# Kernel tuning notes

Measured on AMD Instinct MI355X. Metric: run time of the kernel, lower is better.

Reference implementation:

```python
import math
import jax, jax.numpy as jnp
from jax import lax
import numpy as np

B, Q, D, H = 64, 512, 128, 256
KS, BLOCKS = 3, 2
PI = math.pi

def _ln(x, w, b):
    m = x.mean(-1, keepdims=True)
    v = ((x - m) ** 2).mean(-1, keepdims=True)
    return (x - m) / jnp.sqrt(v + 1e-5) * w + b

def _conv1d(x, w, b, dil):
    # x: (B, C, L), w: (O, I, K), replicate ('edge') padding as in torch padding_mode='replicate'
    pad = (w.shape[-1] - 1) * dil // 2
    xp = jnp.pad(x, ((0, 0), (0, 0), (pad, pad)), mode='edge')
    y = lax.conv_general_dilated(xp, w, (1,), 'VALID', rhs_dilation=(dil,),
                                 dimension_numbers=('NCH', 'OIH', 'NCH'))
    return y + b[None, :, None]

def _rotate(x, rho, phi):
    M = x.shape[-1] // 2
    re, im = x[:, :M], x[:, M:]
    c, s = jnp.cos(phi), jnp.sin(phi)
    return jnp.concatenate([rho * (c * re - s * im), rho * (s * re + c * im)], axis=1)

def setup_inputs():
    key = jax.random.key(0)
    ks = iter(jax.random.split(key, 40))
    def nrm(shape, scale=0.05):
        return jax.random.normal(next(ks), shape, dtype=jnp.float32) * scale
    inp = {}
    inp['x_in'] = jax.random.normal(next(ks), (B, Q, D), dtype=jnp.float32)
    inp['w_out'] = 64
    inp['inp_w'] = nrm((H, 3 * D, 1)); inp['inp_b'] = jnp.zeros((H,), jnp.float32)
    for i in range(BLOCKS):
        inp['blk%d_c1_w' % i] = nrm((H, H, KS)); inp['blk%d_c1_b' % i] = jnp.zeros((H,), jnp.float32)
        inp['blk%d_c2_w' % i] = nrm((H, H, KS)); inp['blk%d_c2_b' % i] = jnp.zeros((H,), jnp.float32)
        inp['blk%d_ln_w' % i] = jnp.ones((H,), jnp.float32); inp['blk%d_ln_b' % i] = jnp.zeros((H,), jnp.float32)
    inp['out_ln_w'] = jnp.ones((H,), jnp.float32); inp['out_ln_b'] = jnp.zeros((H,), jnp.float32)
    inp['fc_gain_w'] = nrm((D, H)); inp['fc_gain_b'] = jnp.zeros((D,), jnp.float32)
    inp['fc_rp_w'] = nrm((2, H)); inp['fc_rp_b'] = jnp.zeros((2,), jnp.float32)
    inp['roll_in_w'] = nrm((H, H + D)); inp['roll_in_b'] = jnp.zeros((H,), jnp.float32)
    inp['gru_w_ih'] = nrm((3 * H, H)); inp['gru_w_hh'] = nrm((3 * H, H))
    inp['gru_b_ih'] = jnp.zeros((3 * H,), jnp.float32); inp['gru_b_hh'] = jnp.zeros((3 * H,), jnp.float32)
    inp['roll_ln_w'] = jnp.ones((H,), jnp.float32); inp['roll_ln_b'] = jnp.zeros((H,), jnp.float32)
    inp['fc_rp_r_w'] = nrm((2, H)); inp['fc_rp_r_b'] = jnp.zeros((2,), jnp.float32)
    return inp

def reference(x_in, w_out, inp_w, inp_b,
              blk0_c1_w, blk0_c1_b, blk0_c2_w, blk0_c2_b, blk0_ln_w, blk0_ln_b,
              blk1_c1_w, blk1_c1_b, blk1_c2_w, blk1_c2_b, blk1_ln_w, blk1_ln_b,
              out_ln_w, out_ln_b, fc_gain_w, fc_gain_b, fc_rp_w, fc_rp_b,
              roll_in_w, roll_in_b, gru_w_ih, gru_w_hh, gru_b_ih, gru_b_hh,
              roll_ln_w, roll_ln_b, fc_rp_r_w, fc_rp_r_b):
    # ---- feature construction: [y, dy, ddy] with dy[0]=ddy[0]=0, ddy[1]=dy[1]
    dy = jnp.concatenate([jnp.zeros_like(x_in[:, :1]), x_in[:, 1:] - x_in[:, :-1]], axis=1)
    ddy = jnp.concatenate([jnp.zeros_like(dy[:, :1]), dy[:, 1:] - dy[:, :-1]], axis=1)
    feats = jnp.concatenate([x_in, dy, ddy], axis=-1)  # (B, q, 3D)
    # ---- TCN encoder (eval mode: dropout = identity)
    h = _conv1d(feats.transpose(0, 2, 1), inp_w, inp_b, 1)  # (B, H, q)
    blks = [(blk0_c1_w, blk0_c1_b, blk0_c2_w, blk0_c2_b, blk0_ln_w, blk0_ln_b, 1),
            (blk1_c1_w, blk1_c1_b, blk1_c2_w, blk1_c2_b, blk1_ln_w, blk1_ln_b, 2)]
    for c1w, c1b, c2w, c2b, lnw, lnb, dil in blks:
        y = jax.nn.gelu(_conv1d(h, c1w, c1b, dil), approximate=False)
        y = jax.nn.gelu(_conv1d(y, c2w, c2b, dil), approximate=False)
        h = _ln((h + y).transpose(0, 2, 1), lnw, lnb).transpose(0, 2, 1)
    h_seq = _ln(h.transpose(0, 2, 1), out_ln_w, out_ln_b)  # (B, q, H)
    # ---- Kalman-style rotate/gain recurrence over q steps
    def kstep(x_post, inputs):
        y_t, h_t = inputs
        rp = h_t @ fc_rp_w.T + fc_rp_b
        rho = jax.nn.sigmoid(rp[:, 0:1]) * 1.25
        phi = PI * jnp.tanh(rp[:, 1:2])
        x_pri = _rotate(x_post, rho, phi)
        Kg = jax.nn.sigmoid(h_t @ fc_gain_w.T + fc_gain_b)
        return x_pri + Kg * (y_t - x_pri), None
    x_post, _ = lax.scan(kstep, x_in[:, 0, :],
                         (x_in.transpose(1, 0, 2), h_seq.transpose(1, 0, 2)))
    # ---- GRU rollout for w_out steps (torch GRUCell gate order: r|z|n)
    def gru(zx, hh):
        gi = zx @ gru_w_ih.T + gru_b_ih
        gh = hh @ gru_w_hh.T + gru_b_hh
        ir, iz, inn = jnp.split(gi, 3, axis=-1)
        hr, hz, hn = jnp.split(gh, 3, axis=-1)
        r = jax.nn.sigmoid(ir + hr)
        zg = jax.nn.sigmoid(iz + hz)
        n = jnp.tanh(inn + r * hn)
        return (1.0 - zg) * n + zg * hh
    def rstep(carry, _):
        h_r, curr = carry
        z = jnp.tanh(jnp.concatenate([h_r, curr], axis=1) @ roll_in_w.T + roll_in_b)
        h_r = _ln(gru(z, h_r), roll_ln_w, roll_ln_b)
        rp = h_r @ fc_rp_r_w.T + fc_rp_r_b
        rho = jax.nn.sigmoid(rp[:, 0:1]) * 1.25
        phi = PI * jnp.tanh(rp[:, 1:2])
        curr = _rotate(curr, rho, phi)
        return (h_r, curr), curr
    _, preds = lax.scan(rstep, (h_seq[:, -1, :], x_post), None, length=w_out)
    return preds.transpose(1, 0, 2)  # (B, w_out, D)
```

## Files before the change

### kernel.cpp

```cpp
#include <hip/hip_runtime.h>
#include <math.h>

#define QLEN 512
#define NB   64
#define DD   128
#define HH   256
#define WOUT 64
#define PI_F 3.14159265358979323846f

typedef __attribute__((ext_vector_type(8))) short bf16x8;
typedef __attribute__((ext_vector_type(4))) float f32x4;

__device__ __forceinline__ float sigmf(float x){ return 1.0f/(1.0f+expf(-x)); }
__device__ __forceinline__ float geluf(float x){ return 0.5f*x*(1.0f+erff(x*0.7071067811865476f)); }

__device__ __forceinline__ unsigned short f2bf(float f){
    unsigned u = __float_as_uint(f);
    u += 0x7fffu + ((u >> 16) & 1u);
    return (unsigned short)(u >> 16);
}
__device__ __forceinline__ float bf2f(unsigned short h){
    return __uint_as_float(((unsigned)h) << 16);
}

__device__ __forceinline__ void packw_elem(const float* __restrict__ w,
                                           unsigned short* __restrict__ dst,
                                           int idx, int CIN, int COUT, int KS) {
    int j = idx & 7; int rest = idx >> 3;
    int lane = rest & 63; rest >>= 6;
    int NT = COUT >> 4;
    int nt = rest % NT; int kt = rest / NT;
    int k = kt*32 + (lane >> 4)*8 + j;
    int cout = nt*16 + (lane & 15);
    int tap = k / CIN, ci = k - tap*CIN;
    float v = w[((size_t)cout*CIN + ci)*KS + tap];
    unsigned short h0 = f2bf(v);  float r = v - bf2f(h0);
    unsigned short h1 = f2bf(r);  r -= bf2f(h1);
    unsigned short h2 = f2bf(r);
    int SZ = KS*CIN*COUT;
    dst[idx] = h0; dst[SZ + idx] = h1; dst[2*SZ + idx] = h2;
}
__device__ __forceinline__ void pq_elem(const float* __restrict__ in,
                                        float4* __restrict__ out,
                                        int idx, int R, int C) {
    int r = idx % R, j4 = idx / R;
    const float* p = in + (size_t)r*C + 4*j4;
    float4 v; v.x = p[0]; v.y = p[1]; v.z = p[2]; v.w = p[3];
    out[idx] = v;
}
__global__ __launch_bounds__(256) void prep_k(
    const float* __restrict__ inp_w, const float* __restrict__ b0c1w,
    const float* __restrict__ b0c2w, const float* __restrict__ b1c1w,
    const float* __restrict__ b1c2w, const float* __restrict__ gainw,
    const float* __restrict__ riw,  const float* __restrict__ wih,
    const float* __restrict__ whh,
    unsigned short* __restrict__ Pinp,  unsigned short* __restrict__ Pb0c1,
    unsigned short* __restrict__ Pb0c2, unsigned short* __restrict__ Pb1c1,
    unsigned short* __restrict__ Pb1c2, unsigned short* __restrict__ Pgain,
    float4* __restrict__ Wri4, float4* __restrict__ Wih4, float4* __restrict__ Whh4)
{
    int idx = blockIdx.x*256 + threadIdx.x;
    if      (idx <   98304) packw_elem(inp_w, Pinp,  idx,          384, 256, 1);
    else if (idx <  294912) packw_elem(b0c1w, Pb0c1, idx -  98304, 256, 256, 3);
    else if (idx <  491520) packw_elem(b0c2w, Pb0c2, idx - 294912, 256, 256, 3);
    else if (idx <  688128) packw_elem(b1c1w, Pb1c1, idx - 491520, 256, 256, 3);
    else if (idx <  884736) packw_elem(b1c2w, Pb1c2, idx - 688128, 256, 256, 3);
    else if (idx <  917504) packw_elem(gainw, Pgain, idx - 884736, 256, 128, 1);
    else if (idx <  942080) pq_elem(riw, Wri4, idx - 917504, 256, 384);
    else if (idx <  991232) pq_elem(wih, Wih4, idx - 942080, 768, 256);
    else if (idx < 1040384) pq_elem(whh, Whh4, idx - 991232, 768, 256);
}

template<int CIN, int COUT, int KS, int DIL, int ACT, int FEATS, int TM>
__global__ __launch_bounds__(256, 2) void conv_mfma_k(
    const float* __restrict__ X, const unsigned short* __restrict__ W,
    const float* __restrict__ bias, float* __restrict__ Y)
{
    constexpr int HALO = (KS == 3) ? DIL : 0;
    constexpr int ROWS = TM + 2*HALO;
    constexpr int CINP = CIN + 8;
    constexpr int MF   = TM/16;
    constexpr int NF   = COUT/64;
    constexpr int KT   = (KS*CIN)/32;
    constexpr int TPC  = CIN/32;
    constexpr int WSZ  = KS*CIN*COUT;

    __shared__ __align__(16) unsigned short As[3][ROWS][CINP];

    const int b   = blockIdx.y;
    const int t0  = blockIdx.x * TM;
    const int tid = threadIdx.x;

    if constexpr (FEATS) {
        for (int idx = tid; idx < TM*DD; idx += 256) {
            int r = idx >> 7, d = idx & (DD-1);
            int t = t0 + r;
            const float* xr = X + ((size_t)b*QLEN + t)*DD + d;
            float x    = xr[0];
            float xm1  = (t >= 1) ? xr[-DD]   : 0.f;
            float xm2  = (t >= 2) ? xr[-2*DD] : 0.f;
            float dy   = (t >= 1) ? (x - xm1)   : 0.f;
            float dym1 = (t >= 2) ? (xm1 - xm2) : 0.f;
            float ddy  = (t >= 1) ? (dy - dym1) : 0.f;
            float vals[3] = {x, dy, ddy};
            #pragma unroll
            for (int f = 0; f < 3; ++f) {
                float v = vals[f];
                unsigned short h0 = f2bf(v);  float rr = v - bf2f(h0);
                unsigned short h1 = f2bf(rr); rr -= bf2f(h1);
                unsigned short h2 = f2bf(rr);
                As[0][r][f*DD + d] = h0;
                As[1][r][f*DD + d] = h1;
                As[2][r][f*DD + d] = h2;
            }
        }
    } else {
        for (int idx = tid; idx < ROWS*(CIN/4); idx += 256) {
            int r = idx / (CIN/4), c4 = idx % (CIN/4);
            int gr = t0 + r - HALO;
            gr = gr < 0 ? 0 : (gr > QLEN-1 ? QLEN-1 : gr);
            float4 v = reinterpret_cast<const float4*>(X + ((size_t)b*QLEN + gr)*CIN)[c4];
            float vv[4] = {v.x, v.y, v.z, v.w};
            ushort4 s0, s1, s2;
            unsigned short* q0 = (unsigned short*)&s0;
            unsigned short* q1 = (unsigned short*)&s1;
            unsigned short* q2 = (unsigned short*)&s2;
            #pragma unroll
            for (int e = 0; e < 4; ++e) {
                float v1 = vv[e];
                unsigned short h0 = f2bf(v1);  float rr = v1 - bf2f(h0);
                unsigned short h1 = f2bf(rr);  rr -= bf2f(h1);
                q0[e] = h0; q1[e] = h1; q2[e] = f2bf(rr);
            }
            *reinterpret_cast<ushort4*>(&As[0][r][c4*4]) = s0;
            *reinterpret_cast<ushort4*>(&As[1][r][c4*4]) = s1;
            *reinterpret_cast<ushort4*>(&As[2][r][c4*4]) = s2;
        }
    }
    __syncthreads();

    const int wv = tid >> 6, l = tid & 63;
    const int lr = l & 15, lk = l >> 4;

    f32x4 acc[MF][NF];
    #pragma unroll
    for (int m = 0; m < MF; ++m)
        #pragma unroll
        for (int n = 0; n < NF; ++n)
            #pragma unroll
            for (int i = 0; i < 4; ++i) acc[m][n][i] = 0.f;

    auto loadB = [&](int kt, bf16x8 (&Bf)[NF][3]) {
        #pragma unroll
        for (int n = 0; n < NF; ++n) {
            const unsigned short* p =
                W + ((size_t)(kt*(COUT/16) + wv*NF + n)*64 + l)*8;
            #pragma unroll
            for (int q = 0; q < 3; ++q)
                Bf[n][q] = *reinterpret_cast<const bf16x8*>(p + (size_t)q*WSZ);
        }
    };
    auto comp = [&](int kt, bf16x8 (&Bf)[NF][3]) {
        const int tap = kt / TPC;
        const int kin = (kt % TPC)*32 + lk*8;
        bf16x8 A[MF][3];
        #pragma unroll
        for (int m = 0; m < MF; ++m) {
            const int row = m*16 + lr + tap*DIL;
            #pragma unroll
            for (int q = 0; q < 3; ++q)
                A[m][q] = *reinterpret_cast<const bf16x8*>(&As[q][row][kin]);
        }
        #pragma unroll
        for (int m = 0; m < MF; ++m)
            #pragma unroll
            for (int n = 0; n < NF; ++n) {
                f32x4 c = acc[m][n];
                c = __builtin_amdgcn_mfma_f32_16x16x32_bf16(A[m][0], Bf[n][0], c, 0,0,0);
                c = __builtin_amdgcn_mfma_f32_16x16x32_bf16(A[m][0], Bf[n][1], c, 0,0,0);
                c = __builtin_amdgcn_mfma_f32_16x16x32_bf16(A[m][1], Bf[n][0], c, 0,0,0);
                c = __builtin_amdgcn_mfma_f32_16x16x32_bf16(A[m][0], Bf[n][2], c, 0,0,0);
                c = __builtin_amdgcn_mfma_f32_16x16x32_bf16(A[m][1], Bf[n][1], c, 0,0,0);
                c = __builtin_amdgcn_mfma_f32_16x16x32_bf16(A[m][2], Bf[n][0], c, 0,0,0);
                acc[m][n] = c;
            }
    };

    bf16x8 B0[NF][3], B1[NF][3];
    loadB(0, B0);
    #pragma unroll 1
    for (int kt = 0; kt < KT; kt += 2) {
        loadB(kt+1, B1);
        comp(kt, B0);
        if (kt + 2 < KT) loadB(kt+2, B0);
        comp(kt+1, B1);
    }

    #pragma unroll
    for (int n = 0; n < NF; ++n) {
        const int col = (wv*NF + n)*16 + lr;
        const float bv = bias[col];
        #pragma unroll
        for (int m = 0; m < MF; ++m) {
            #pragma unroll
            for (int i = 0; i < 4; ++i) {
                float v = acc[m][n][i] + bv;
                if constexpr (ACT == 1) v = geluf(v);
                if constexpr (ACT == 2) v = sigmf(v);
                Y[((size_t)b*QLEN + t0 + m*16 + lk*4 + i)*COUT + col] = v;
            }
        }
    }
}

__global__ __launch_bounds__(256) void ln_k(
    const float* __restrict__ X, const float* __restrict__ R,
    const float* __restrict__ w, const float* __restrict__ b,
    float* __restrict__ Y)
{
    int row  = blockIdx.x*4 + (threadIdx.x >> 6);
    int lane = threadIdx.x & 63;
    float4 v = reinterpret_cast<const float4*>(X + (size_t)row*HH)[lane];
    float4 rv = reinterpret_cast<const float4*>(R + (size_t)row*HH)[lane];
    v.x += rv.x; v.y += rv.y; v.z += rv.z; v.w += rv.w;
    float s = v.x + v.y + v.z + v.w;
    #pragma unroll
    for (int off = 32; off > 0; off >>= 1) s += __shfl_xor(s, off);
    float m = s * (1.0f/HH);
    float dx=v.x-m, dy=v.y-m, dz=v.z-m, dw=v.w-m;
    float q = dx*dx + dy*dy + dz*dz + dw*dw;
    #pragma unroll
    for (int off = 32; off > 0; off >>= 1) q += __shfl_xor(q, off);
    float inv = rsqrtf(q*(1.0f/HH) + 1e-5f);
    float4 wv = reinterpret_cast<const float4*>(w)[lane];
    float4 bv = reinterpret_cast<const float4*>(b)[lane];
    float4 o;
    o.x = dx*inv*wv.x + bv.x;
    o.y = dy*inv*wv.y + bv.y;
    o.z = dz*inv*wv.z + bv.z;
    o.w = dw*inv*wv.w + bv.w;
    reinterpret_cast<float4*>(Y + (size_t)row*HH)[lane] = o;
}

__global__ __launch_bounds__(256) void ln_rp_k(
    const float* __restrict__ X, const float* __restrict__ w, const float* __restrict__ b,
    const float* __restrict__ rpw, const float* __restrict__ rpb,
    float* __restrict__ Y, float* __restrict__ rho, float* __restrict__ phi)
{
    int row  = blockIdx.x*4 + (threadIdx.x >> 6);
    int lane = threadIdx.x & 63;
    float4 v = reinterpret_cast<const float4*>(X + (size_t)row*HH)[lane];
    float s = v.x + v.y + v.z + v.w;
    #pragma unroll
    for (int off = 32; off > 0; off >>= 1) s += __shfl_xor(s, off);
    float m = s * (1.0f/HH);
    float dx=v.x-m, dy=v.y-m, dz=v.z-m, dw=v.w-m;
    float q = dx*dx + dy*dy + dz*dz + dw*dw;
    #pragma unroll
    for (int off = 32; off > 0; off >>= 1) q += __shfl_xor(q, off);
    float inv = rsqrtf(q*(1.0f/HH) + 1e-5f);
    float4 wv = reinterpret_cast<const float4*>(w)[lane];
    float4 bv = reinterpret_cast<const float4*>(b)[lane];
    float4 o;
    o.x = dx*inv*wv.x + bv.x;
    o.y = dy*inv*wv.y + bv.y;
    o.z = dz*inv*wv.z + bv.z;
    o.w = dw*inv*wv.w + bv.w;
    reinterpret_cast<float4*>(Y + (size_t)row*HH)[lane] = o;

    float4 w0 = reinterpret_cast<const float4*>(rpw)[lane];
    float4 w1 = reinterpret_cast<const float4*>(rpw + HH)[lane];
    float d0 = o.x*w0.x + o.y*w0.y + o.z*w0.z + o.w*w0.w;
    float d1 = o.x*w1.x + o.y*w1.y + o.z*w1.z + o.w*w1.w;
    #pragma unroll
    for (int off = 32; off > 0; off >>= 1) { d0 += __shfl_xor(d0, off); d1 += __shfl_xor(d1, off); }
    if (lane == 0) {
        rho[row] = 1.25f * sigmf(d0 + rpb[0]);
        phi[row] = PI_F * tanhf(d1 + rpb[1]);
    }
}

__global__ __launch_bounds__(64) void kalman_k(
    const float* __restrict__ Xin, const float* __restrict__ Kg,
    const float* __restrict__ rho_a, const float* __restrict__ phi_a,
    float* __restrict__ xpost)
{
    int b = blockIdx.x, l = threadIdx.x;
    const float* xb = Xin + (size_t)b*QLEN*DD;
    float re = xb[l], im = xb[64 + l];

    float rho_c = rho_a[b*QLEN], phi_c = phi_a[b*QLEN];
    const float* kg0 = Kg + (size_t)b*QLEN*DD;
    float kr_c = kg0[l], ki_c = kg0[64 + l];
    float y0_c = xb[l],  y1_c = xb[64 + l];

    for (int t = 0; t < QLEN; ++t) {
        float rho_n = 0.f, phi_n = 0.f, kr_n = 0.f, ki_n = 0.f, y0_n = 0.f, y1_n = 0.f;
        if (t + 1 < QLEN) {
            rho_n = rho_a[b*QLEN + t + 1];
            phi_n = phi_a[b*QLEN + t + 1];
            const float* kg = Kg + ((size_t)b*QLEN + t + 1)*DD;
            const float* yr = xb + (size_t)(t + 1)*DD;
            kr_n = kg[l]; ki_n = kg[64 + l];
            y0_n = yr[l]; y1_n = yr[64 + l];
        }
        float sn, cs; sincosf(phi_c, &sn, &cs);
        float pr = rho_c*(cs*re - sn*im);
        float pi = rho_c*(sn*re + cs*im);
        re = pr + kr_c*(y0_c - pr);
        im = pi + ki_c*(y1_c - pi);
        rho_c = rho_n; phi_c = phi_n; kr_c = kr_n; ki_c = ki_n; y0_c = y0_n; y1_c = y1_n;
    }
    xpost[b*DD + l]      = re;
    xpost[b*DD + 64 + l] = im;
}

__device__ __forceinline__ float bsum16(float v, float* red) {
    #pragma unroll
    for (int off = 32; off > 0; off >>= 1) v += __shfl_xor(v, off);
    __syncthreads();
    if ((threadIdx.x & 63) == 0) red[threadIdx.x >> 6] = v;
    __syncthreads();
    float s = 0.f;
    #pragma unroll
    for (int i = 0; i < 16; ++i) s += red[i];
    return s;
}
__device__ __forceinline__ float2 bsum16_2(float a, float b, float* red) {
    #pragma unroll
    for (int off = 32; off > 0; off >>= 1) { a += __shfl_xor(a, off); b += __shfl_xor(b, off); }
    __syncthreads();
    if ((threadIdx.x & 63) == 0) { red[threadIdx.x >> 6] = a; red[16 + (threadIdx.x >> 6)] = b; }
    __syncthreads();
    float sa = 0.f, sb = 0.f;
    #pragma unroll
    for (int i = 0; i < 16; ++i) { sa += red[i]; sb += red[16 + i]; }
    float2 r; r.x = sa; r.y = sb; return r;
}

__global__ __launch_bounds__(1024) void rollout_k5(
    const float* __restrict__ Hs, const float* __restrict__ xpost,
    const float4* __restrict__ Wri4,
    const float* __restrict__ rib,
    const float4* __restrict__ Wih4,
    const float4* __restrict__ Whh4,
    const float* __restrict__ bih, const float* __restrict__ bhh,
    const float* __restrict__ lnw, const float* __restrict__ lnb,
    const float* __restrict__ rpw, const float* __restrict__ rpb,
    float* __restrict__ out)
{
    __shared__ __align__(16) float hc[384];
    __shared__ __align__(16) float zsh[256];
    __shared__ float zpart[4][256];
    __shared__ float gpart[6][4][256];
    __shared__ float red[32];

    const int tid = threadIdx.x;
    const int o = tid & 255, p = tid >> 8;
    const int b = blockIdx.x;

    if (p == 0) hc[o] = Hs[((size_t)b*QLEN + QLEN-1)*HH + o];
    if (p == 1 && o < DD) hc[HH + o] = xpost[b*DD + o];

    const float bi0 = bih[o],    bi1 = bih[HH+o], bi2 = bih[2*HH+o];
    const float bh0 = bhh[o],    bh1 = bhh[HH+o], bh2 = bhh[2*HH+o];
    const float rb  = rib[o];
    const float lw  = lnw[o],    lb  = lnb[o];
    const float rw0 = rpw[o],    rw1 = rpw[HH+o];
    const float rpb0 = rpb[0],   rpb1 = rpb[1];
    const float4* hc4 = reinterpret_cast<const float4*>(hc);
    const float4* zf4 = reinterpret_cast<const float4*>(zsh);
    __syncthreads();

    for (int s = 0; s < WOUT; ++s) {
        float az = 0.f;
        {
            const float4* wp = Wri4 + (size_t)(p*24)*256 + o;
            #pragma unroll 8
            for (int j4 = 0; j4 < 24; ++j4) {
                float4 w = wp[(size_t)j4*256];
                float4 h = hc4[p*24 + j4];
                az = fmaf(w.x, h.x, az); az = fmaf(w.y, h.y, az);
                az = fmaf(w.z, h.z, az); az = fmaf(w.w, h.w, az);
            }
        }
        float e0=0.f, e1=0.f, e2=0.f;
        {
            const float4* whp = Whh4 + (size_t)(p*16)*768 + o;
            #pragma unroll 4
            for (int j4 = 0; j4 < 16; ++j4) {
                float4 h = hc4[p*16 + j4];
                float4 wd = whp[(size_t)j4*768];
                float4 we = whp[(size_t)j4*768 + 256];
                float4 wf = whp[(size_t)j4*768 + 512];
                e0 = fmaf(wd.x,h.x,e0); e0 = fmaf(wd.y,h.y,e0); e0 = fmaf(wd.z,h.z,e0); e0 = fmaf(wd.w,h.w,e0);
                e1 = fmaf(we.x,h.x,e1); e1 = fmaf(we.y,h.y,e1); e1 = fmaf(we.z,h.z,e1); e1 = fmaf(we.w,h.w,e1);
                e2 = fmaf(wf.x,h.x,e2); e2 = fmaf(wf.y,h.y,e2); e2 = fmaf(wf.z,h.z,e2); e2 = fmaf(wf.w,h.w,e2);
            }
        }
        zpart[p][o] = az;
        gpart[3][p][o]=e0; gpart[4][p][o]=e1; gpart[5][p][o]=e2;
        __syncthreads();
        if (p == 0)
            zsh[o] = tanhf(zpart[0][o]+zpart[1][o]+zpart[2][o]+zpart[3][o] + rb);
        __syncthreads();

        float g0=0.f, g1=0.f, g2=0.f;
        {
            const float4* wip = Wih4 + (size_t)(p*16)*768 + o;
            #pragma unroll 4
            for (int j4 = 0; j4 < 16; ++j4) {
                float4 z = zf4[p*16 + j4];
                float4 wa = wip[(size_t)j4*768];
                float4 wb = wip[(size_t)j4*768 + 256];
                float4 wc = wip[(size_t)j4*768 + 512];
                g0 = fmaf(wa.x,z.x,g0); g0 = fmaf(wa.y,z.y,g0); g0 = fmaf(wa.z,z.z,g0); g0 = fmaf(wa.w,z.w,g0);
                g1 = fmaf(wb.x,z.x,g1); g1 = fmaf(wb.y,z.y,g1); g1 = fmaf(wb.z,z.z,g1); g1 = fmaf(wb.w,z.w,g1);
                g2 = fmaf(wc.x,z.x,g2); g2 = fmaf(wc.y,z.y,g2); g2 = fmaf(wc.z,z.z,g2); g2 = fmaf(wc.w,z.w,g2);
            }
        }
        gpart[0][p][o]=g0; gpart[1][p][o]=g1; gpart[2][p][o]=g2;
        __syncthreads();

        float go = 0.f;
        if (p == 0) {
            float G0 = gpart[0][0][o]+gpart[0][1][o]+gpart[0][2][o]+gpart[0][3][o] + bi0;
            float G1 = gpart[1][0][o]+gpart[1][1][o]+gpart[1][2][o]+gpart[1][3][o] + bi1;
            float G2 = gpart[2][0][o]+gpart[2][1][o]+gpart[2][2][o]+gpart[2][3][o] + bi2;
            float E0 = gpart[3][0][o]+gpart[3][1][o]+gpart[3][2][o]+gpart[3][3][o] + bh0;
            float E1 = gpart[4][0][o]+gpart[4][1][o]+gpart[4][2][o]+gpart[4][3][o] + bh1;
            float E2 = gpart[5][0][o]+gpart[5][1][o]+gpart[5][2][o]+gpart[5][3][o] + bh2;
            float r  = sigmf(G0 + E0);
            float zg = sigmf(G1 + E1);
            float n  = tanhf(G2 + r*E2);
            go = (1.0f - zg)*n + zg*hc[o];
        }

        float m   = bsum16(go, red) * (1.0f/HH);
        float d   = (p == 0) ? (go - m) : 0.f;
        float var = bsum16(d*d, red) * (1.0f/HH);
        float hn  = (p == 0) ? (d * rsqrtf(var + 1e-5f) * lw + lb) : 0.f;

        float2 ps = bsum16_2((p == 0) ? hn*rw0 : 0.f, (p == 0) ? hn*rw1 : 0.f, red);
        float rho = 1.25f * sigmf(ps.x + rpb0);
        float phi = PI_F * tanhf(ps.y + rpb1);
        float sn, cs; sincosf(phi, &sn, &cs);

        if (p == 0) hc[o] = hn;
        if (tid < 64) {
            float cre = hc[HH + tid], cim = hc[HH + 64 + tid];
            float nr = rho*(cs*cre - sn*cim);
            float ni = rho*(sn*cre + cs*cim);
            hc[HH + tid] = nr; hc[HH + 64 + tid] = ni;
            float* ob = out + ((size_t)b*WOUT + s)*DD;
            ob[tid] = nr; ob[64 + tid] = ni;
        }
        __syncthreads();
    }
}

extern "C" void kernel_launch(void* const* d_in, const int* in_sizes, int n_in,
                              void* d_out, int out_size, void* d_ws, size_t ws_size,
                              hipStream_t stream)
{
    const float* x_in   = (const float*)d_in[0];
    const float* inp_w  = (const float*)d_in[2];
    const float* inp_b  = (const float*)d_in[3];
    const float* b0c1w  = (const float*)d_in[4];
    const float* b0c1b  = (const float*)d_in[5];
    const float* b0c2w  = (const float*)d_in[6];
    const float* b0c2b  = (const float*)d_in[7];
    const float* b0lnw  = (const float*)d_in[8];
    const float* b0lnb  = (const float*)d_in[9];
    const float* b1c1w  = (const float*)d_in[10];
    const float* b1c1b  = (const float*)d_in[11];
    const float* b1c2w  = (const float*)d_in[12];
    const float* b1c2b  = (const float*)d_in[13];
    const float* b1lnw  = (const float*)d_in[14];
    const float* b1lnb  = (const float*)d_in[15];
    const float* olnw   = (const float*)d_in[16];
    const float* olnb   = (const float*)d_in[17];
    const float* gainw  = (const float*)d_in[18];
    const float* gainb  = (const float*)d_in[19];
    const float* rpw    = (const float*)d_in[20];
    const float* rpb    = (const float*)d_in[21];
    const float* riw    = (const float*)d_in[22];
    const float* rib    = (const float*)d_in[23];
    const float* wih    = (const float*)d_in[24];
    const float* whh    = (const float*)d_in[25];
    const float* bih    = (const float*)d_in[26];
    const float* bhh    = (const float*)d_in[27];
    const float* rlnw   = (const float*)d_in[28];
    const float* rlnb   = (const float*)d_in[29];
    const float* rprw   = (const float*)d_in[30];
    const float* rprb   = (const float*)d_in[31];
    float* out = (float*)d_out;

    float* ws   = (float*)d_ws;
    float* buf0 = ws;
    float* buf1 = ws +  8388608;
    float* buf2 = ws + 16777216;
    float* Kg    = buf2;
    float* rhoA  = buf2 + 4194304;
    float* phiA  = rhoA + 32768;
    float* xpost = phiA + 32768;
    float* wts   = ws + 25165824;
    unsigned short* Pinp  = (unsigned short*)wts;
    unsigned short* Pb0c1 = Pinp  + 294912;
    unsigned short* Pb0c2 = Pb0c1 + 589824;
    unsigned short* Pb1c1 = Pb0c2 + 589824;
    unsigned short* Pb1c2 = Pb1c1 + 589824;
    unsigned short* Pgain = Pb1c2 + 589824;
    float4* Wri4 = (float4*)(wts + 1376256);
    float4* Wih4 = (float4*)(wts + 1376256 +  98304);
    float4* Whh4 = (float4*)(wts + 1376256 + 294912);

    prep_k<<<4064, 256, 0, stream>>>(inp_w, b0c1w, b0c2w, b1c1w, b1c2w, gainw,
                                     riw, wih, whh,
                                     Pinp, Pb0c1, Pb0c2, Pb1c1, Pb1c2, Pgain,
                                     Wri4, Wih4, Whh4);

    dim3 cg16(QLEN/16, NB);
    dim3 cg32(QLEN/32, NB);

    conv_mfma_k<384,256,1,1,0,1,16><<<cg16, 256, 0, stream>>>(x_in, Pinp, inp_b, buf0);

    conv_mfma_k<256,256,3,1,1,0,32><<<cg32, 256, 0, stream>>>(buf0, Pb0c1, b0c1b, buf1);
    conv_mfma_k<256,256,3,1,1,0,32><<<cg32, 256, 0, stream>>>(buf1, Pb0c2, b0c2b, buf2);
    ln_k<<<NB*QLEN/4, 256, 0, stream>>>(buf0, buf2, b0lnw, b0lnb, buf1);

    conv_mfma_k<256,256,3,2,1,0,32><<<cg32, 256, 0, stream>>>(buf1, Pb1c1, b1c1b, buf0);
    conv_mfma_k<256,256,3,2,1,0,32><<<cg32, 256, 0, stream>>>(buf0, Pb1c2, b1c2b, buf2);
    ln_k<<<NB*QLEN/4, 256, 0, stream>>>(buf1, buf2, b1lnw, b1lnb, buf0);

    ln_rp_k<<<NB*QLEN/4, 256, 0, stream>>>(buf0, olnw, olnb, rpw, rpb,
                                           buf1, rhoA, phiA);

    conv_mfma_k<256,128,1,1,2,0,32><<<cg32, 256, 0, stream>>>(buf1, Pgain, gainb, Kg);

    kalman_k<<<NB, 64, 0, stream>>>(x_in, Kg, rhoA, phiA, xpost);

    rollout_k5<<<NB, 1024, 0, stream>>>(buf1, xpost, Wri4, rib, Wih4, Whh4,
                                        bih, bhh, rlnw, rlnb, rprw, rprb, out);
}
```

Baseline: 1.714 ms.

## Split GRU rollout across 128 blocks with LDS-resident weight slices and grid barriers

The rollout kernel previously ran one block per batch row and streamed all GRU and input-projection weights from global memory on every step. It now uses 4 groups of 32 blocks. Each block keeps an 8-output slice of the weights in shared memory and serves 16 batch rows, exchanging z and raw h through global buffers. Software grid barriers built on atomic counters (zeroed in prep_k) synchronise each group twice per step. This removes the repeated weight traffic, but it depends on all 128 blocks being co-resident and adds global-barrier latency on every one of the 64 steps.

Result: slower. 2.299 ms (+34.1%).

```diff
diff --git a/kernel.cpp b/kernel.cpp
--- a/kernel.cpp
+++ b/kernel.cpp
@@ -40,24 +40,14 @@
     int SZ = KS*CIN*COUT;
     dst[idx] = h0; dst[SZ + idx] = h1; dst[2*SZ + idx] = h2;
 }
-__device__ __forceinline__ void pq_elem(const float* __restrict__ in,
-                                        float4* __restrict__ out,
-                                        int idx, int R, int C) {
-    int r = idx % R, j4 = idx / R;
-    const float* p = in + (size_t)r*C + 4*j4;
-    float4 v; v.x = p[0]; v.y = p[1]; v.z = p[2]; v.w = p[3];
-    out[idx] = v;
-}
 __global__ __launch_bounds__(256) void prep_k(
     const float* __restrict__ inp_w, const float* __restrict__ b0c1w,
     const float* __restrict__ b0c2w, const float* __restrict__ b1c1w,
     const float* __restrict__ b1c2w, const float* __restrict__ gainw,
-    const float* __restrict__ riw,  const float* __restrict__ wih,
-    const float* __restrict__ whh,
     unsigned short* __restrict__ Pinp,  unsigned short* __restrict__ Pb0c1,
     unsigned short* __restrict__ Pb0c2, unsigned short* __restrict__ Pb1c1,
     unsigned short* __restrict__ Pb1c2, unsigned short* __restrict__ Pgain,
-    float4* __restrict__ Wri4, float4* __restrict__ Wih4, float4* __restrict__ Whh4)
+    unsigned* __restrict__ bars)
 {
     int idx = blockIdx.x*256 + threadIdx.x;
     if      (idx <   98304) packw_elem(inp_w, Pinp,  idx,          384, 256, 1);
@@ -66,9 +56,7 @@
     else if (idx <  688128) packw_elem(b1c1w, Pb1c1, idx - 491520, 256, 256, 3);
     else if (idx <  884736) packw_elem(b1c2w, Pb1c2, idx - 688128, 256, 256, 3);
     else if (idx <  917504) packw_elem(gainw, Pgain, idx - 884736, 256, 128, 1);
-    else if (idx <  942080) pq_elem(riw, Wri4, idx - 917504, 256, 384);
-    else if (idx <  991232) pq_elem(wih, Wih4, idx - 942080, 768, 256);
-    else if (idx < 1040384) pq_elem(whh, Whh4, idx - 991232, 768, 256);
+    else if (idx <  917632) bars[idx - 917504] = 0u;
 }
 
 template<int CIN, int COUT, int KS, int DIL, int ACT, int FEATS, int TM>
@@ -315,147 +303,198 @@
     xpost[b*DD + 64 + l] = im;
 }
 
-__device__ __forceinline__ float bsum16(float v, float* red) {
-    #pragma unroll
-    for (int off = 32; off > 0; off >>= 1) v += __shfl_xor(v, off);
+#define GBLK 32
+#define BPG  16
+#define ZSL  8
+#define GSL  24
+
+__device__ __forceinline__ void gbar(unsigned* cnt, unsigned target) {
     __syncthreads();
-    if ((threadIdx.x & 63) == 0) red[threadIdx.x >> 6] = v;
+    if (threadIdx.x == 0) {
+        unsigned a = __hip_atomic_fetch_add(cnt, 1u, __ATOMIC_ACQ_REL, __HIP_MEMORY_SCOPE_AGENT);
+        if (a != target - 1u) {
+            while (__hip_atomic_load(cnt, __ATOMIC_ACQUIRE, __HIP_MEMORY_SCOPE_AGENT) < target)
+                __builtin_amdgcn_s_sleep(2);
+        }
+    }
     __syncthreads();
-    float s = 0.f;
-    #pragma unroll
-    for (int i = 0; i < 16; ++i) s += red[i];
-    return s;
-}
-__device__ __forceinline__ float2 bsum16_2(float a, float b, float* red) {
-    #pragma unroll
-    for (int off = 32; off > 0; off >>= 1) { a += __shfl_xor(a, off); b += __shfl_xor(b, off); }
-    __syncthreads();
-    if ((threadIdx.x & 63) == 0) { red[threadIdx.x >> 6] = a; red[16 + (threadIdx.x >> 6)] = b; }
-    __syncthreads();
-    float sa = 0.f, sb = 0.f;
-    #pragma unroll
-    for (int i = 0; i < 16; ++i) { sa += red[i]; sb += red[16 + i]; }
-    float2 r; r.x = sa; r.y = sb; return r;
-}
-
-__global__ __launch_bounds__(1024) void rollout_k5(
+}
+
+__global__ __launch_bounds__(1024) void rollout_k7(
     const float* __restrict__ Hs, const float* __restrict__ xpost,
-    const float4* __restrict__ Wri4,
-    const float* __restrict__ rib,
-    const float4* __restrict__ Wih4,
-    const float4* __restrict__ Whh4,
+    const float* __restrict__ riw, const float* __restrict__ rib,
+    const float* __restrict__ wih, const float* __restrict__ whh,
     const float* __restrict__ bih, const float* __restrict__ bhh,
     const float* __restrict__ lnw, const float* __restrict__ lnb,
     const float* __restrict__ rpw, const float* __restrict__ rpb,
-    float* __restrict__ out)
-{
-    __shared__ __align__(16) float hc[384];
-    __shared__ __align__(16) float zsh[256];
-    __shared__ float zpart[4][256];
-    __shared__ float gpart[6][4][256];
-    __shared__ float red[32];
+    float* __restrict__ zbuf, float* __restrict__ hraw,
+    unsigned* __restrict__ bars, float* __restrict__ out)
+{
+    __shared__ __align__(16) float Wri_s[ZSL][388];
+    __shared__ __align__(16) float Wih_s[GSL][260];
+    __shared__ __align__(16) float Whh_s[GSL][260];
+    __shared__ __align__(16) float hcs[BPG][388];
+    __shared__ __align__(16) float sbuf[BPG][260];
+    __shared__ float ghs[GSL][BPG];
+    __shared__ float gis[GSL][BPG];
+    __shared__ float lnw_s[256], lnb_s[256], rw0_s[256], rw1_s[256];
 
     const int tid = threadIdx.x;
-    const int o = tid & 255, p = tid >> 8;
-    const int b = blockIdx.x;
-
-    if (p == 0) hc[o] = Hs[((size_t)b*QLEN + QLEN-1)*HH + o];
-    if (p == 1 && o < DD) hc[HH + o] = xpost[b*DD + o];
-
-    const float bi0 = bih[o],    bi1 = bih[HH+o], bi2 = bih[2*HH+o];
-    const float bh0 = bhh[o],    bh1 = bhh[HH+o], bh2 = bhh[2*HH+o];
-    const float rb  = rib[o];
-    const float lw  = lnw[o],    lb  = lnb[o];
-    const float rw0 = rpw[o],    rw1 = rpw[HH+o];
-    const float rpb0 = rpb[0],   rpb1 = rpb[1];
-    const float4* hc4 = reinterpret_cast<const float4*>(hc);
-    const float4* zf4 = reinterpret_cast<const float4*>(zsh);
+    const int g   = blockIdx.x >> 5;
+    const int j   = blockIdx.x & 31;
+    const int o0  = j * ZSL;
+    const int b0  = g * BPG;
+    unsigned* bcnt = bars + g*32;
+
+    for (int i = tid; i < ZSL*384; i += 1024) {
+        int r = i / 384, k = i - r*384;
+        Wri_s[r][k] = riw[(size_t)(o0 + r)*384 + k];
+    }
+    for (int i = tid; i < GSL*256; i += 1024) {
+        int r = i >> 8, k = i & 255;
+        int gate = r >> 3, oo = r & 7;
+        size_t grow = (size_t)(gate*256 + o0 + oo)*256 + k;
+        Wih_s[r][k] = wih[grow];
+        Whh_s[r][k] = whh[grow];
+    }
+    if (tid < 256) {
+        lnw_s[tid] = lnw[tid]; lnb_s[tid] = lnb[tid];
+        rw0_s[tid] = rpw[tid]; rw1_s[tid] = rpw[256 + tid];
+    }
+    for (int i = tid; i < BPG*256; i += 1024) {
+        int b = i >> 8, c = i & 255;
+        hcs[b][c] = Hs[((size_t)(b0 + b)*QLEN + (QLEN-1))*HH + c];
+    }
+    for (int i = tid; i < BPG*128; i += 1024) {
+        int b = i >> 7, c = i & 127;
+        hcs[b][256 + c] = xpost[(b0 + b)*DD + c];
+    }
+
+    const int zoo = tid & 7, zb2 = tid >> 3;
+    const int u   = tid - 64;
+    const int gbt = (u >= 0) ? (u / 24) : 0;
+    const int gr  = (u >= 0) ? (u - gbt*24) : 0;
+    const int bbt = tid / 24, br = tid - bbt*24;
+    float ribv = 0.f, bhhv = 0.f, bihv = 0.f;
+    if (tid < 64)               ribv = rib[o0 + zoo];
+    if (tid >= 64 && tid < 160) bhhv = bhh[(gr >> 3)*256 + o0 + (gr & 7)];
+    if (tid < 96)               bihv = bih[(br >> 3)*256 + o0 + (br & 7)];
+    const float rpb0 = rpb[0], rpb1 = rpb[1];
     __syncthreads();
 
-    for (int s = 0; s < WOUT; ++s) {
-        float az = 0.f;
+    unsigned nbar = 0;
+
+    for (int s = 0; ; ++s) {
+        if (s > 0) {
+            {
+                int b = tid >> 6, c4 = tid & 63;
+                *reinterpret_cast<float4*>(&sbuf[b][c4*4]) =
+                    *reinterpret_cast<const float4*>(hraw + (size_t)(b0 + b)*256 + c4*4);
+            }
+            __syncthreads();
+            {
+                const int b = tid >> 6, l = tid & 63;
+                float4 v = *reinterpret_cast<const float4*>(&sbuf[b][l*4]);
+                float sm = v.x + v.y + v.z + v.w;
+                #pragma unroll
+                for (int off = 32; off > 0; off >>= 1) sm += __shfl_xor(sm, off);
+                float m = sm * (1.0f/HH);
+                float dx=v.x-m, dy=v.y-m, dz=v.z-m, dw=v.w-m;
+                float q = dx*dx + dy*dy + dz*dz + dw*dw;
+                #pragma unroll
+                for (int off = 32; off > 0; off >>= 1) q += __shfl_xor(q, off);
+                float inv = rsqrtf(q*(1.0f/HH) + 1e-5f);
+                float h0 = dx*inv*lnw_s[l*4+0] + lnb_s[l*4+0];
+                float h1 = dy*inv*lnw_s[l*4+1] + lnb_s[l*4+1];
+                float h2 = dz*inv*lnw_s[l*4+2] + lnb_s[l*4+2];
+                float h3 = dw*inv*lnw_s[l*4+3] + lnb_s[l*4+3];
+                float4 hv; hv.x=h0; hv.y=h1; hv.z=h2; hv.w=h3;
+                *reinterpret_cast<float4*>(&hcs[b][l*4]) = hv;
+                float d0 = h0*rw0_s[l*4+0] + h1*rw0_s[l*4+1] + h2*rw0_s[l*4+2] + h3*rw0_s[l*4+3];
+                float d1 = h0*rw1_s[l*4+0] + h1*rw1_s[l*4+1] + h2*rw1_s[l*4+2] + h3*rw1_s[l*4+3];
+                #pragma unroll
+                for (int off = 32; off > 0; off >>= 1) { d0 += __shfl_xor(d0, off); d1 += __shfl_xor(d1, off); }
+                float rho = 1.25f * sigmf(d0 + rpb0);
+                float phi = PI_F * tanhf(d1 + rpb1);
+                float sn, cs; sincosf(phi, &sn, &cs);
+                float re = hcs[b][256 + l], im = hcs[b][320 + l];
+                float nr = rho*(cs*re - sn*im);
+                float ni = rho*(sn*re + cs*im);
+                hcs[b][256 + l] = nr; hcs[b][320 + l] = ni;
+                if (j == b) {
+                    float* ob = out + ((size_t)(b0 + b)*WOUT + (s-1))*DD;
+                    ob[l] = nr; ob[64 + l] = ni;
+                }
+            }
+            __syncthreads();
+            if (s == WOUT) break;
+        }
+
+        if (tid < 64) {
+            const int bb = zb2*2;
+            float a0 = 0.f, a1 = 0.f;
+            for (int kq = 0; kq < 96; ++kq) {
+                float4 w  = *reinterpret_cast<const float4*>(&Wri_s[zoo][kq*4]);
+                float4 x0 = *reinterpret_cast<const float4*>(&hcs[bb  ][kq*4]);
+                float4 x1 = *reinterpret_cast<const float4*>(&hcs[bb+1][kq*4]);
+                a0 = fmaf(w.x,x0.x,a0); a0 = fmaf(w.y,x0.y,a0); a0 = fmaf(w.z,x0.z,a0); a0 = fmaf(w.w,x0.w,a0);
+                a1 = fmaf(w.x,x1.x,a1); a1 = fmaf(w.y,x1.y,a1); a1 = fmaf(w.z,x1.z,a1); a1 = fmaf(w.w,x1.w,a1);
+            }
+            zbuf[(size_t)(b0+bb  )*256 + o0 + zoo] = tanhf(a0 + ribv);
+            zbuf[(size_t)(b0+bb+1)*256 + o0 + zoo] = tanhf(a1 + ribv);
+        } else if (tid < 160) {
+            const int bb = gbt*4;
+            float a0=0.f, a1=0.f, a2=0.f, a3=0.f;
+            for (int kq = 0; kq < 64; ++kq) {
+                float4 w  = *reinterpret_cast<const float4*>(&Whh_s[gr][kq*4]);
+                float4 x0 = *reinterpret_cast<const float4*>(&hcs[bb+0][kq*4]);
+                float4 x1 = *reinterpret_cast<const float4*>(&hcs[bb+1][kq*4]);
+                float4 x2 = *reinterpret_cast<const float4*>(&hcs[bb+2][kq*4]);
+                float4 x3 = *reinterpret_cast<const float4*>(&hcs[bb+3][kq*4]);
+                a0 = fmaf(w.x,x0.x,a0); a0 = fmaf(w.y,x0.y,a0); a0 = fmaf(w.z,x0.z,a0); a0 = fmaf(w.w,x0.w,a0);
+                a1 = fmaf(w.x,x1.x,a1); a1 = fmaf(w.y,x1.y,a1); a1 = fmaf(w.z,x1.z,a1); a1 = fmaf(w.w,x1.w,a1);
+                a2 = fmaf(w.x,x2.x,a2); a2 = fmaf(w.y,x2.y,a2); a2 = fmaf(w.z,x2.z,a2); a2 = fmaf(w.w,x2.w,a2);
+                a3 = fmaf(w.x,x3.x,a3); a3 = fmaf(w.y,x3.y,a3); a3 = fmaf(w.z,x3.z,a3); a3 = fmaf(w.w,x3.w,a3);
+            }
+            ghs[gr][bb+0] = a0 + bhhv; ghs[gr][bb+1] = a1 + bhhv;
+            ghs[gr][bb+2] = a2 + bhhv; ghs[gr][bb+3] = a3 + bhhv;
+        }
+        nbar++; gbar(bcnt, nbar*GBLK);
+
         {
-            const float4* wp = Wri4 + (size_t)(p*24)*256 + o;
-            #pragma unroll 8
-            for (int j4 = 0; j4 < 24; ++j4) {
-                float4 w = wp[(size_t)j4*256];
-                float4 h = hc4[p*24 + j4];
-                az = fmaf(w.x, h.x, az); az = fmaf(w.y, h.y, az);
-                az = fmaf(w.z, h.z, az); az = fmaf(w.w, h.w, az);
-            }
-        }
-        float e0=0.f, e1=0.f, e2=0.f;
-        {
-            const float4* whp = Whh4 + (size_t)(p*16)*768 + o;
-            #pragma unroll 4
-            for (int j4 = 0; j4 < 16; ++j4) {
-                float4 h = hc4[p*16 + j4];
-                float4 wd = whp[(size_t)j4*768];
-                float4 we = whp[(size_t)j4*768 + 256];
-                float4 wf = whp[(size_t)j4*768 + 512];
-                e0 = fmaf(wd.x,h.x,e0); e0 = fmaf(wd.y,h.y,e0); e0 = fmaf(wd.z,h.z,e0); e0 = fmaf(wd.w,h.w,e0);
-                e1 = fmaf(we.x,h.x,e1); e1 = fmaf(we.y,h.y,e1); e1 = fmaf(we.z,h.z,e1); e1 = fmaf(we.w,h.w,e1);
-                e2 = fmaf(wf.x,h.x,e2); e2 = fmaf(wf.y,h.y,e2); e2 = fmaf(wf.z,h.z,e2); e2 = fmaf(wf.w,h.w,e2);
-            }
-        }
-        zpart[p][o] = az;
-        gpart[3][p][o]=e0; gpart[4][p][o]=e1; gpart[5][p][o]=e2;
+            int b = tid >> 6, c4 = tid & 63;
+            *reinterpret_cast<float4*>(&sbuf[b][c4*4]) =
+                *reinterpret_cast<const float4*>(zbuf + (size_t)(b0 + b)*256 + c4*4);
+        }
         __syncthreads();
-        if (p == 0)
-            zsh[o] = tanhf(zpart[0][o]+zpart[1][o]+zpart[2][o]+zpart[3][o] + rb);
+        if (tid < 96) {
+            const int bb = bbt*4;
+            float a0=0.f, a1=0.f, a2=0.f, a3=0.f;
+            for (int kq = 0; kq < 64; ++kq) {
+                float4 w  = *reinterpret_cast<const float4*>(&Wih_s[br][kq*4]);
+                float4 x0 = *reinterpret_cast<const float4*>(&sbuf[bb+0][kq*4]);
+                float4 x1 = *reinterpret_cast<const float4*>(&sbuf[bb+1][kq*4]);
+                float4 x2 = *reinterpret_cast<const float4*>(&sbuf[bb+2][kq*4]);
+                float4 x3 = *reinterpret_cast<const float4*>(&sbuf[bb+3][kq*4]);
+                a0 = fmaf(w.x,x0.x,a0); a0 = fmaf(w.y,x0.y,a0); a0 = fmaf(w.z,x0.z,a0); a0 = fmaf(w.w,x0.w,a0);
+                a1 = fmaf(w.x,x1.x,a1); a1 = fmaf(w.y,x1.y,a1); a1 = fmaf(w.z,x1.z,a1); a1 = fmaf(w.w,x1.w,a1);
+                a2 = fmaf(w.x,x2.x,a2); a2 = fmaf(w.y,x2.y,a2); a2 = fmaf(w.z,x2.z,a2); a2 = fmaf(w.w,x2.w,a2);
+                a3 = fmaf(w.x,x3.x,a3); a3 = fmaf(w.y,x3.y,a3); a3 = fmaf(w.z,x3.z,a3); a3 = fmaf(w.w,x3.w,a3);
+            }
+            gis[br][bb+0] = a0 + bihv; gis[br][bb+1] = a1 + bihv;
+            gis[br][bb+2] = a2 + bihv; gis[br][bb+3] = a3 + bihv;
+        }
         __syncthreads();
-
-        float g0=0.f, g1=0.f, g2=0.f;
-        {
-            const float4* wip = Wih4 + (size_t)(p*16)*768 + o;
-            #pragma unroll 4
-            for (int j4 = 0; j4 < 16; ++j4) {
-                float4 z = zf4[p*16 + j4];
-                float4 wa = wip[(size_t)j4*768];
-                float4 wb = wip[(size_t)j4*768 + 256];
-                float4 wc = wip[(size_t)j4*768 + 512];
-                g0 = fmaf(wa.x,z.x,g0); g0 = fmaf(wa.y,z.y,g0); g0 = fmaf(wa.z,z.z,g0); g0 = fmaf(wa.w,z.w,g0);
-                g1 = fmaf(wb.x,z.x,g1); g1 = fmaf(wb.y,z.y,g1); g1 = fmaf(wb.z,z.z,g1); g1 = fmaf(wb.w,z.w,g1);
-                g2 = fmaf(wc.x,z.x,g2); g2 = fmaf(wc.y,z.y,g2); g2 = fmaf(wc.z,z.z,g2); g2 = fmaf(wc.w,z.w,g2);
-            }
-        }
-        gpart[0][p][o]=g0; gpart[1][p][o]=g1; gpart[2][p][o]=g2;
-        __syncthreads();
-
-        float go = 0.f;
-        if (p == 0) {
-            float G0 = gpart[0][0][o]+gpart[0][1][o]+gpart[0][2][o]+gpart[0][3][o] + bi0;
-            float G1 = gpart[1][0][o]+gpart[1][1][o]+gpart[1][2][o]+gpart[1][3][o] + bi1;
-            float G2 = gpart[2][0][o]+gpart[2][1][o]+gpart[2][2][o]+gpart[2][3][o] + bi2;
-            float E0 = gpart[3][0][o]+gpart[3][1][o]+gpart[3][2][o]+gpart[3][3][o] + bh0;
-            float E1 = gpart[4][0][o]+gpart[4][1][o]+gpart[4][2][o]+gpart[4][3][o] + bh1;
-            float E2 = gpart[5][0][o]+gpart[5][1][o]+gpart[5][2][o]+gpart[5][3][o] + bh2;
+        if (tid < 128) {
+            const int oo = tid & 7, b = tid >> 3;
+            float G0 = gis[oo][b], G1 = gis[8+oo][b], G2 = gis[16+oo][b];
+            float E0 = ghs[oo][b], E1 = ghs[8+oo][b], E2 = ghs[16+oo][b];
             float r  = sigmf(G0 + E0);
             float zg = sigmf(G1 + E1);
             float n  = tanhf(G2 + r*E2);
-            go = (1.0f - zg)*n + zg*hc[o];
-        }
-
-        float m   = bsum16(go, red) * (1.0f/HH);
-        float d   = (p == 0) ? (go - m) : 0.f;
-        float var = bsum16(d*d, red) * (1.0f/HH);
-        float hn  = (p == 0) ? (d * rsqrtf(var + 1e-5f) * lw + lb) : 0.f;
-
-        float2 ps = bsum16_2((p == 0) ? hn*rw0 : 0.f, (p == 0) ? hn*rw1 : 0.f, red);
-        float rho = 1.25f * sigmf(ps.x + rpb0);
-        float phi = PI_F * tanhf(ps.y + rpb1);
-        float sn, cs; sincosf(phi, &sn, &cs);
-
-        if (p == 0) hc[o] = hn;
-        if (tid < 64) {
-            float cre = hc[HH + tid], cim = hc[HH + 64 + tid];
-            float nr = rho*(cs*cre - sn*cim);
-            float ni = rho*(sn*cre + cs*cim);
-            hc[HH + tid] = nr; hc[HH + 64 + tid] = ni;
-            float* ob = out + ((size_t)b*WOUT + s)*DD;
-            ob[tid] = nr; ob[64 + tid] = ni;
-        }
-        __syncthreads();
+            hraw[(size_t)(b0 + b)*256 + o0 + oo] = (1.0f - zg)*n + zg*hcs[b][o0 + oo];
+        }
+        nbar++; gbar(bcnt, nbar*GBLK);
     }
 }
 
@@ -511,14 +550,13 @@
     unsigned short* Pb1c1 = Pb0c2 + 589824;
     unsigned short* Pb1c2 = Pb1c1 + 589824;
     unsigned short* Pgain = Pb1c2 + 589824;
-    float4* Wri4 = (float4*)(wts + 1376256);
-    float4* Wih4 = (float4*)(wts + 1376256 +  98304);
-    float4* Whh4 = (float4*)(wts + 1376256 + 294912);
-
-    prep_k<<<4064, 256, 0, stream>>>(inp_w, b0c1w, b0c2w, b1c1w, b1c2w, gainw,
-                                     riw, wih, whh,
+    float* zbufp = wts + 1376256;
+    float* hrawp = zbufp + 16384;
+    unsigned* barsp = (unsigned*)(hrawp + 16384);
+
+    prep_k<<<3585, 256, 0, stream>>>(inp_w, b0c1w, b0c2w, b1c1w, b1c2w, gainw,
                                      Pinp, Pb0c1, Pb0c2, Pb1c1, Pb1c2, Pgain,
-                                     Wri4, Wih4, Whh4);
+                                     barsp);
 
     dim3 cg16(QLEN/16, NB);
     dim3 cg32(QLEN/32, NB);
@@ -540,6 +578,7 @@
 
     kalman_k<<<NB, 64, 0, stream>>>(x_in, Kg, rhoA, phiA, xpost);
 
-    rollout_k5<<<NB, 1024, 0, stream>>>(buf1, xpost, Wri4, rib, Wih4, Whh4,
-                                        bih, bhh, rlnw, rlnb, rprw, rprb, out);
-}
+    rollout_k7<<<128, 1024, 0, stream>>>(buf1, xpost, riw, rib, wih, whh,
+                                         bih, bhh, rlnw, rlnb, rprw, rprb,
+                                         zbufp, hrawp, barsp, out);
+}
```
